# Kernel optimization log

Hardware: AMD Instinct MI355X
Metric: run time of the kernel (lower is better)

## Reference

```python
import math
import jax, jax.numpy as jnp
import numpy as np

D_MODEL = 1024
N_HEAD = 16
HEAD_DIM = D_MODEL // N_HEAD
B, T = 2, 2048


def _layernorm(x, g, b, eps=1e-5):
    mu = jnp.mean(x, axis=-1, keepdims=True)
    var = jnp.mean(jnp.square(x - mu), axis=-1, keepdims=True)
    return (x - mu) * jax.lax.rsqrt(var + eps) * g + b


def _l2norm(x, eps=1e-12):
    n = jnp.sqrt(jnp.sum(jnp.square(x), axis=-1, keepdims=True))
    return x / jnp.maximum(n, eps)


def _rope(x, times):
    # x: [B,T,H,Dh] (Dh even), times: [T]
    half = x.shape[-1] // 2
    freqs = jnp.exp(-jnp.arange(half, dtype=x.dtype) * (math.log(10000.0) / half))
    theta = times[:, None] * freqs[None, :]              # [T, half]
    cos = jnp.cos(theta)[None, :, None, :]               # [1,T,1,half]
    sin = jnp.sin(theta)[None, :, None, :]
    xr = x.reshape(*x.shape[:-1], half, 2)
    x1, x2 = xr[..., 0], xr[..., 1]
    r1 = x1 * cos - x2 * sin
    r2 = x1 * sin + x2 * cos
    return jnp.stack([r1, r2], axis=-1).reshape(x.shape)


def setup_inputs() -> dict:
    key = jax.random.key(0)
    ks = jax.random.split(key, 16)
    s = 0.02
    f32 = jnp.float32
    inp = {
        'x': jax.random.normal(ks[0], (B, T, D_MODEL), f32),
        'Wq': jax.random.normal(ks[1], (D_MODEL, D_MODEL), f32) * s,
        'Wk': jax.random.normal(ks[2], (D_MODEL, D_MODEL), f32) * s,
        'Wv': jax.random.normal(ks[3], (D_MODEL, D_MODEL), f32) * s,
        'gate_w': jax.random.normal(ks[4], (D_MODEL, D_MODEL), f32) * s,
        'gate_b': jnp.zeros((D_MODEL,), f32),
        'p_w': jax.random.normal(ks[5], (D_MODEL, D_MODEL), f32) * s,
        'p_b': jnp.zeros((D_MODEL,), f32),
        'out_w': jax.random.normal(ks[6], (D_MODEL, D_MODEL), f32) * s,
        'out_b': jnp.zeros((D_MODEL,), f32),
        'clock_w': jax.random.normal(ks[7], (D_MODEL, N_HEAD), f32) * s,
        'clock_b': jnp.zeros((N_HEAD,), f32),
        'ln1_g': jnp.ones((D_MODEL,), f32), 'ln1_b': jnp.zeros((D_MODEL,), f32),
        'ln2_g': jnp.ones((D_MODEL,), f32), 'ln2_b': jnp.zeros((D_MODEL,), f32),
        'mlp_w1': jax.random.normal(ks[8], (D_MODEL, 4 * D_MODEL), f32) * s,
        'mlp_b1': jnp.zeros((4 * D_MODEL,), f32),
        'mlp_w2': jax.random.normal(ks[9], (4 * D_MODEL, D_MODEL), f32) * s,
        'mlp_b2': jnp.zeros((D_MODEL,), f32),
    }
    return inp


def reference(x, Wq, Wk, Wv, gate_w, gate_b, p_w, p_b, out_w, out_b,
              clock_w, clock_b, ln1_g, ln1_b, ln2_g, ln2_b,
              mlp_w1, mlp_b1, mlp_w2, mlp_b2):
    Bx, Tx, D = x.shape
    H, Dh = N_HEAD, HEAD_DIM
    residual = x
    xn = _layernorm(x, ln1_g, ln1_b)
    times = jnp.arange(Tx, dtype=x.dtype)

    q = _l2norm((xn @ Wq).reshape(Bx, Tx, H, Dh))
    k = _l2norm((xn @ Wk).reshape(Bx, Tx, H, Dh))
    v = (xn @ Wv).reshape(Bx, Tx, H, Dh)
    clock = jax.nn.softplus(xn @ clock_w + clock_b).reshape(Bx, Tx, H, 1)

    q = _rope(q, times)
    k = _rope(k, times)

    gj = -jax.nn.softplus(xn @ gate_w + gate_b).reshape(Bx, Tx, H, Dh)
    gcp = jnp.exp(jnp.clip(jnp.cumsum(gj, axis=1), -60.0, 50.0))
    q = q * gcp
    k = k / (gcp + 1e-8)

    p = (xn @ p_w + p_b).reshape(Bx, Tx, H, Dh)
    p_max = jnp.max(p, axis=1, keepdims=True)
    p_exp = jnp.exp(p - p_max) * clock
    p_cs = jnp.cumsum(p_exp, axis=1)
    q = q / (p_cs + 1e-8)
    k = k * p_exp

    # causal softmax attention (SDPA, scale = 1/sqrt(Dh))
    scores = jnp.einsum('bqhd,bkhd->bhqk', q, k) / math.sqrt(Dh)
    mask = jnp.tril(jnp.ones((Tx, Tx), dtype=bool))
    scores = jnp.where(mask[None, None], scores, -jnp.inf)
    attn = jax.nn.softmax(scores, axis=-1)
    out = jnp.einsum('bhqk,bkhd->bqhd', attn, v).reshape(Bx, Tx, D)

    out = out @ out_w + out_b
    x1 = out + residual
    h = _layernorm(x1, ln2_g, ln2_b)
    h = jax.nn.gelu(h @ mlp_w1 + mlp_b1, approximate=False) @ mlp_w2 + mlp_b2
    return x1 + h
```

## Files before the change

### kernel.cpp

```cpp
#include <hip/hip_runtime.h>
#include <hip/hip_bf16.h>
#include <math.h>

typedef __hip_bfloat16 bf16;
typedef __attribute__((ext_vector_type(8))) short short8;
typedef __attribute__((ext_vector_type(4))) short short4v;
typedef __attribute__((ext_vector_type(4))) float f32x4;

#define BT   4096
#define DM   1024
#define NH   16
#define DH   64
#define TSEQ 2048

__device__ __forceinline__ float wave_sum(float v){
#pragma unroll
  for (int o = 32; o; o >>= 1) v += __shfl_xor(v, o);
  return v;
}

__device__ __forceinline__ float block_sum(float v){
  __shared__ float sm[4];
  v = wave_sum(v);
  __syncthreads();
  if ((threadIdx.x & 63) == 0) sm[threadIdx.x >> 6] = v;
  __syncthreads();
  return sm[0] + sm[1] + sm[2] + sm[3];
}

__device__ __forceinline__ float softplusf(float x){
  return x > 20.f ? x : __logf(1.f + __expf(x));
}

__device__ __forceinline__ short f2bf(float f){
  unsigned u = __builtin_bit_cast(unsigned, f);
  u += 0x7FFF + ((u >> 16) & 1);
  return (short)(u >> 16);
}

__device__ __forceinline__ short8 ld8(const short* p){
  short4v a = *(const short4v*)p;
  short4v b = *(const short4v*)(p + 4);
  short8 r;
  r[0]=a[0]; r[1]=a[1]; r[2]=a[2]; r[3]=a[3];
  r[4]=b[0]; r[5]=b[1]; r[6]=b[2]; r[7]=b[3];
  return r;
}

__device__ __forceinline__ void async16(const short* g, short* l){
  __builtin_amdgcn_global_load_lds(
      (const __attribute__((address_space(1))) void*)g,
      (__attribute__((address_space(3))) void*)l, 16, 0, 0);
}

__device__ __forceinline__ int xcd_swizzle(int lin, int nwg){
  const int q = nwg >> 3, r = nwg & 7;
  const int xcd = lin & 7, i = lin >> 3;
  return (xcd < r ? xcd * (q + 1) : r * (q + 1) + (xcd - r) * q) + i;
}

__device__ __forceinline__ void wt_body(const float* __restrict__ src,
    short* __restrict__ dst, int K, int N){
  __shared__ short T[32][33];
  const int tx = threadIdx.x & 31, ty = threadIdx.x >> 5;
  const int n0 = blockIdx.x << 5, k0 = blockIdx.y << 5;
#pragma unroll
  for (int r = 0; r < 4; r++){
    const int k = k0 + (ty << 2) + r;
    const int n = n0 + tx;
    T[tx][(ty << 2) + r] = (n < N) ? f2bf(src[(long)k * N + n]) : (short)0;
  }
  __syncthreads();
#pragma unroll
  for (int r = 0; r < 4; r++){
    const int n = n0 + (ty << 2) + r;
    if (n < N) dst[(long)n * K + k0 + tx] = T[(ty << 2) + r][tx];
  }
}

__global__ __launch_bounds__(256) void wt_kernel(const float* __restrict__ src,
    short* __restrict__ dst, int K, int N){
  wt_body(src, dst, K, N);
}

__global__ __launch_bounds__(256) void wt6_kernel(
    const float* s0, const float* s1, const float* s2, const float* s3,
    const float* s4, const float* s5,
    short* d0, short* d1, short* d2, short* d3, short* d4, short* d5){
  const float* src; short* dst;
  switch (blockIdx.z){
    case 0: src = s0; dst = d0; break;
    case 1: src = s1; dst = d1; break;
    case 2: src = s2; dst = d2; break;
    case 3: src = s3; dst = d3; break;
    case 4: src = s4; dst = d4; break;
    default: src = s5; dst = d5; break;
  }
  wt_body(src, dst, DM, DM);
}

__global__ __launch_bounds__(256) void biascat_fill(const float* __restrict__ gb,
    const float* __restrict__ pb, const float* __restrict__ cb, float* __restrict__ out){
  const int i = blockIdx.x * 256 + threadIdx.x;
  if (i >= 5136) return;
  float v = 0.f;
  if (i >= 5120) v = cb[i - 5120];
  else if (i >= 4096) v = pb[i - 4096];
  else if (i >= 3072) v = gb[i - 3072];
  out[i] = v;
}

__global__ __launch_bounds__(256) void ln_kernel(const float* __restrict__ xin,
    const float* __restrict__ g, const float* __restrict__ bb, short* __restrict__ out){
  const long row = blockIdx.x;
  const int tid = threadIdx.x;
  float v[4];
#pragma unroll
  for (int i = 0; i < 4; i++) v[i] = xin[row * DM + tid + i * 256];
  float s = block_sum(v[0] + v[1] + v[2] + v[3]);
  const float mu = s * (1.f / DM);
  float d2 = 0.f;
#pragma unroll
  for (int i = 0; i < 4; i++){ float dd = v[i] - mu; d2 = fmaf(dd, dd, d2); }
  d2 = block_sum(d2);
  const float rstd = rsqrtf(d2 * (1.f / DM) + 1e-5f);
#pragma unroll
  for (int i = 0; i < 4; i++){
    int c = tid + i * 256;
    out[row * DM + c] = f2bf(fmaf((v[i] - mu) * rstd, g[c], bb[c]));
  }
}

template <int EPI>
__global__ __launch_bounds__(256) void gemm_bt(
    const short* __restrict__ A, const short* __restrict__ Bt,
    const float* __restrict__ bias, const float* __restrict__ resf,
    const float* __restrict__ bias2, float* __restrict__ Cf2,
    float* __restrict__ Cf, short* __restrict__ Cbf, int M, int N, int K)
{
  __shared__ __attribute__((aligned(16))) short As[3][4096];
  __shared__ __attribute__((aligned(16))) short Bs[3][4096];
  const int tid = threadIdx.x;
  const int lane = tid & 63, w = tid >> 6;
  const int l16 = lane & 15, quad = lane >> 4;
  const int wm = w >> 1, wn = w & 1;
  const int gx = (int)gridDim.x, gy = (int)gridDim.y;
  int wg = xcd_swizzle((int)blockIdx.x + gx * ((int)blockIdx.y + gy * (int)blockIdx.z),
                       gx * gy * (int)gridDim.z);
  const int bx = wg % gx; wg /= gx;
  const int by = wg % gy; wg /= gy;
  const int bz = wg;
  const int bm0 = by << 7, bn0 = bx << 7;
  const int ks = K / (int)gridDim.z;
  const int kbeg = bz * ks;
  const int nt = ks >> 5;

  const int csw = (tid >> 3) & 3;
  const int r0 = tid >> 2,        c0 = (tid & 3) ^ csw;
  const int r1 = 64 + (tid >> 2);
  const short* ga0 = A  + (long)(bm0 + r0) * K + kbeg + c0 * 8;
  const short* ga1 = A  + (long)(bm0 + r1) * K + kbeg + c0 * 8;
  const short* gb0 = Bt + (long)min(bn0 + r0, N - 1) * K + kbeg + c0 * 8;
  const short* gb1 = Bt + (long)min(bn0 + r1, N - 1) * K + kbeg + c0 * 8;
  const int wofs = w << 9;

#define STAGE(buf, t) do {                                   \
    const long ko_ = (long)(t) * 32;                         \
    async16(ga0 + ko_, &As[buf][wofs]);                      \
    async16(gb0 + ko_, &Bs[buf][wofs]);                      \
    async16(ga1 + ko_, &As[buf][2048 + wofs]);               \
    async16(gb1 + ko_, &Bs[buf][2048 + wofs]);               \
  } while (0)

  f32x4 acc[4][4] = {};

  STAGE(0, 0);
  if (nt > 1) STAGE(1, 1);

  const int qsw = (quad ^ ((l16 >> 1) & 3)) * 8;

  int cur = 0, stg = 2;
  for (int t = 0; t < nt; t++){
    if (t + 1 < nt){
      asm volatile("s_waitcnt vmcnt(4)" ::: "memory");
    } else {
      asm volatile("s_waitcnt vmcnt(0)" ::: "memory");
    }
    __builtin_amdgcn_s_barrier();
    __builtin_amdgcn_sched_barrier(0);
    if (t + 2 < nt) STAGE(stg, t + 2);
    short8 af[4], bfr[4];
#pragma unroll
    for (int i = 0; i < 4; i++){
      af[i]  = *(const short8*)&As[cur][(wm * 64 + i * 16 + l16) * 32 + qsw];
      bfr[i] = *(const short8*)&Bs[cur][(wn * 64 + i * 16 + l16) * 32 + qsw];
    }
#pragma unroll
    for (int i = 0; i < 4; i++)
#pragma unroll
      for (int j = 0; j < 4; j++)
        acc[i][j] = __builtin_amdgcn_mfma_f32_16x16x32_bf16(af[i], bfr[j], acc[i][j], 0, 0, 0);
    cur = (cur == 2) ? 0 : cur + 1;
    stg = (stg == 2) ? 0 : stg + 1;
  }
#undef STAGE

#pragma unroll
  for (int i = 0; i < 4; i++){
#pragma unroll
    for (int r = 0; r < 4; r++){
      const int row = bm0 + wm * 64 + i * 16 + quad * 4 + r;
#pragma unroll
      for (int j = 0; j < 4; j++){
        const int col = bn0 + wn * 64 + j * 16 + l16;
        if (col < N){
          float v = acc[i][j][r];
          const long off = (long)row * N + col;
          if constexpr (EPI >= 1 && EPI != 6) v += bias[col];
          if constexpr (EPI == 2 || EPI == 4) v += resf[off];
          if constexpr (EPI == 3){
            v = 0.5f * v * (1.f + erff(v * 0.70710678118654752f));
            Cbf[off] = f2bf(v);
          } else if constexpr (EPI == 4){
            Cf[off] = v;
            Cf2[off] = v + bias2[col];
          } else if constexpr (EPI == 5){
            if (col < 5120)
              Cf[(long)(col >> 10) * 4194304 + (long)row * 1024 + (col & 1023)] = v;
            else
              Cf[20971520 + (long)row * 16 + (col - 5120)] = v;
          } else if constexpr (EPI == 6){
            unsafeAtomicAdd(&Cf[off], v);
          } else {
            Cf[off] = v;
          }
        }
      }
    }
  }
}

__global__ __launch_bounds__(256) void scan_p1(float* __restrict__ G, const float* __restrict__ P,
    const float* __restrict__ Vf, short* __restrict__ Vh,
    float* __restrict__ cmax, float* __restrict__ gsum){
  const int tid = blockIdx.x * 256 + threadIdx.x;
  const int d = tid & 63, c = (tid >> 6) & 31, bh = tid >> 11;
  const int h = bh & 15, b = bh >> 4;
  const long base = (((long)(b * TSEQ + c * 64)) * NH + h) * 64 + d;
  float mx = -1e30f, gs = 0.f;
  for (int tt = 0; tt < 64; tt++){
    const long idx = base + (long)tt * (NH * 64);
    float gj = -softplusf(G[idx]);
    G[idx] = gj;
    gs += gj;
    mx = fmaxf(mx, P[idx]);
    Vh[idx] = f2bf(Vf[idx]);
  }
  const int chain = bh * 64 + d;
  cmax[chain * 32 + c] = mx;
  gsum[chain * 32 + c] = gs;
}

__global__ void scan_p2(const float* __restrict__ cmax, const float* __restrict__ gsum,
                        float* __restrict__ pmax, float* __restrict__ gpre){
  const int chain = blockIdx.x * 256 + threadIdx.x;
  float mx = -1e30f;
  for (int c = 0; c < 32; c++) mx = fmaxf(mx, cmax[chain * 32 + c]);
  pmax[chain] = mx;
  float run = 0.f;
  for (int c = 0; c < 32; c++){ gpre[chain * 32 + c] = run; run += gsum[chain * 32 + c]; }
}

__global__ __launch_bounds__(256) void scan_p3(const float* __restrict__ G, float* __restrict__ P,
    const float* __restrict__ CLKr, float* __restrict__ Q, float* __restrict__ K,
    const float* __restrict__ pmax, const float* __restrict__ gpre, float* __restrict__ psum){
  const int tid = blockIdx.x * 256 + threadIdx.x;
  const int d = tid & 63, c = (tid >> 6) & 31, bh = tid >> 11;
  const int h = bh & 15, b = bh >> 4;
  const int chain = bh * 64 + d;
  const long base = (((long)(b * TSEQ + c * 64)) * NH + h) * 64 + d;
  const float pm = pmax[chain];
  const float freq = expf(-(float)(d >> 1) * 0.28782313662425575f);
  float sn = sinf((float)(c * 64) * freq);
  float cn = cosf((float)(c * 64) * freq);
  const float sf = sinf(freq), cf = cosf(freq);
  float grun = gpre[chain * 32 + c];
  float ps = 0.f;
  for (int tt = 0; tt < 64; tt++){
    const long idx = base + (long)tt * (NH * 64);
    const int t = c * 64 + tt;
    float clk = softplusf(CLKr[(long)(b * TSEQ + t) * NH + h]);
    float pe = __expf(P[idx] - pm) * clk;
    P[idx] = pe; ps += pe;
    grun += G[idx];
    float gc = __expf(fminf(fmaxf(grun, -60.f), 50.f));
    {
      float q = Q[idx];
      float n = sqrtf(wave_sum(q * q));
      q = q / fmaxf(n, 1e-12f);
      float pr = __shfl_xor(q, 1);
      q = (d & 1) ? fmaf(pr, sn, q * cn) : fmaf(q, cn, -pr * sn);
      Q[idx] = q * gc;
    }
    {
      float k = K[idx];
      float n = sqrtf(wave_sum(k * k));
      k = k / fmaxf(n, 1e-12f);
      float pr = __shfl_xor(k, 1);
      k = (d & 1) ? fmaf(pr, sn, k * cn) : fmaf(k, cn, -pr * sn);
      K[idx] = k / (gc + 1e-8f);
    }
    const float ns = fmaf(sn, cf, cn * sf);
    const float nc = fmaf(cn, cf, -sn * sf);
    sn = ns; cn = nc;
  }
  psum[chain * 32 + c] = ps;
}

__global__ void scan_p4(const float* __restrict__ psum, float* __restrict__ ppre){
  const int chain = blockIdx.x * 256 + threadIdx.x;
  float run = 0.f;
  for (int c = 0; c < 32; c++){ ppre[chain * 32 + c] = run; run += psum[chain * 32 + c]; }
}

__global__ __launch_bounds__(256) void scan_p5(const float* __restrict__ P, const float* __restrict__ Q,
    const float* __restrict__ K, const float* __restrict__ ppre,
    short* __restrict__ Qh, short* __restrict__ Kh){
  const int tid = blockIdx.x * 256 + threadIdx.x;
  const int d = tid & 63, c = (tid >> 6) & 31, bh = tid >> 11;
  const int h = bh & 15, b = bh >> 4;
  const int chain = bh * 64 + d;
  const long base = (((long)(b * TSEQ + c * 64)) * NH + h) * 64 + d;
  float cs = ppre[chain * 32 + c];
  for (int tt = 0; tt < 64; tt++){
    const long idx = base + (long)tt * (NH * 64);
    float pe = P[idx];
    cs += pe;
    Qh[idx] = f2bf(Q[idx] / (cs + 1e-8f) * 0.125f);
    Kh[idx] = f2bf(K[idx] * pe);
  }
}

__global__ __launch_bounds__(256) void fattn_kernel(const short* __restrict__ Qh,
    const short* __restrict__ Kh, const short* __restrict__ Vh, short* __restrict__ O){
  __shared__ __attribute__((aligned(16))) short Ks[64][72];
  __shared__ __attribute__((aligned(16))) short Vt[64][68];
  __shared__ __attribute__((aligned(16))) short Ps[4][16][72];
  const int tid  = threadIdx.x;
  const int lane = tid & 63, w = tid >> 6;
  const int quad = lane >> 4, l16 = lane & 15;
  const int gx = (int)gridDim.x;
  int wgs = xcd_swizzle((int)blockIdx.x + gx * (int)blockIdx.y, gx * (int)gridDim.y);
  const int bxs = wgs % gx;
  const int bh = wgs / gx, h = bh & 15, b = bh >> 4;
  const int qt = gx - 1 - bxs;
  const int q0  = qt << 6;
  const int qw0 = q0 + w * 16;
  const long strideT = NH * DH;
  const long base_bh = ((long)b * TSEQ * NH + h) * DH;

  const short* qp = Qh + base_bh + (long)(qw0 + l16) * strideT + quad * 8;
  const short8 qa0 = *(const short8*)qp;
  const short8 qa1 = *(const short8*)(qp + 32);

  f32x4 oacc[4] = {{0,0,0,0},{0,0,0,0},{0,0,0,0},{0,0,0,0}};
  float lpart[4] = {0.f,0.f,0.f,0.f};

  const int krow = tid >> 2, kcol = (tid & 3) << 4;
  const int vkey = tid & 63, vd0 = (tid >> 6) << 4;
  const short* kbase = Kh + base_bh + (long)krow * strideT + kcol;
  const short* vbase = Vh + base_bh + (long)vkey * strideT + vd0;

  short8 kr0 = *(const short8*)kbase;
  short8 kr1 = *(const short8*)(kbase + 8);
  short8 vr0 = *(const short8*)vbase;
  short8 vr1 = *(const short8*)(vbase + 8);

  const int ntiles = qt + 1;
  for (int t = 0; t < ntiles; t++){
    *(short8*)&Ks[krow][kcol]     = kr0;
    *(short8*)&Ks[krow][kcol + 8] = kr1;
#pragma unroll
    for (int j = 0; j < 8; j++) Vt[vd0 + j][vkey] = vr0[j];
#pragma unroll
    for (int j = 0; j < 8; j++) Vt[vd0 + 8 + j][vkey] = vr1[j];
    __syncthreads();
    if (t + 1 < ntiles){
      const long off = (long)(t + 1) * (64 * strideT);
      kr0 = *(const short8*)(kbase + off);
      kr1 = *(const short8*)(kbase + off + 8);
      vr0 = *(const short8*)(vbase + off);
      vr1 = *(const short8*)(vbase + off + 8);
    }
    const int kt0 = t << 6;
    f32x4 c[4] = {{0,0,0,0},{0,0,0,0},{0,0,0,0},{0,0,0,0}};
#pragma unroll
    for (int kg = 0; kg < 4; kg++){
      const short8 b0 = ld8(&Ks[kg * 16 + l16][quad * 8]);
      const short8 b1 = ld8(&Ks[kg * 16 + l16][32 + quad * 8]);
      c[kg] = __builtin_amdgcn_mfma_f32_16x16x32_bf16(qa0, b0, c[kg], 0, 0, 0);
      c[kg] = __builtin_amdgcn_mfma_f32_16x16x32_bf16(qa1, b1, c[kg], 0, 0, 0);
    }
    if (kt0 + 63 > qw0){
#pragma unroll
      for (int kg = 0; kg < 4; kg++)
#pragma unroll
        for (int r = 0; r < 4; r++){
          const int qq = qw0 + quad * 4 + r;
          if (kt0 + kg * 16 + l16 > qq) c[kg][r] = -1e30f;
        }
    }
#pragma unroll
    for (int kg = 0; kg < 4; kg++)
#pragma unroll
      for (int r = 0; r < 4; r++) c[kg][r] = __expf(c[kg][r] - 0.25f);
#pragma unroll
    for (int r = 0; r < 4; r++)
      lpart[r] += (c[0][r] + c[1][r]) + (c[2][r] + c[3][r]);
#pragma unroll
    for (int kg = 0; kg < 4; kg++)
#pragma unroll
      for (int r = 0; r < 4; r++)
        Ps[w][quad * 4 + r][kg * 16 + l16] = f2bf(c[kg][r]);
    const short8 pa0 = ld8(&Ps[w][l16][quad * 8]);
    const short8 pa1 = ld8(&Ps[w][l16][32 + quad * 8]);
#pragma unroll
    for (int f = 0; f < 4; f++){
      const short8 vb0 = ld8(&Vt[f * 16 + l16][quad * 8]);
      const short8 vb1 = ld8(&Vt[f * 16 + l16][32 + quad * 8]);
      oacc[f] = __builtin_amdgcn_mfma_f32_16x16x32_bf16(pa0, vb0, oacc[f], 0, 0, 0);
      oacc[f] = __builtin_amdgcn_mfma_f32_16x16x32_bf16(pa1, vb1, oacc[f], 0, 0, 0);
    }
    __syncthreads();
  }
#pragma unroll
  for (int r = 0; r < 4; r++){
    float l = lpart[r];
#pragma unroll
    for (int o = 1; o <= 8; o <<= 1) l += __shfl_xor(l, o);
    const float inv = 1.f / l;
    const long row = base_bh + (long)(qw0 + quad * 4 + r) * strideT + l16;
#pragma unroll
    for (int f = 0; f < 4; f++) O[row + f * 16] = f2bf(oacc[f][r] * inv);
  }
}

extern "C" void kernel_launch(void* const* d_in, const int* in_sizes, int n_in,
                              void* d_out, int out_size, void* d_ws, size_t ws_size,
                              hipStream_t stream){
  const float* x       = (const float*)d_in[0];
  const float* Wq      = (const float*)d_in[1];
  const float* Wk      = (const float*)d_in[2];
  const float* Wv      = (const float*)d_in[3];
  const float* gate_w  = (const float*)d_in[4];
  const float* gate_b  = (const float*)d_in[5];
  const float* p_w     = (const float*)d_in[6];
  const float* p_b     = (const float*)d_in[7];
  const float* out_w   = (const float*)d_in[8];
  const float* out_b   = (const float*)d_in[9];
  const float* clock_w = (const float*)d_in[10];
  const float* clock_b = (const float*)d_in[11];
  const float* ln1_g   = (const float*)d_in[12];
  const float* ln1_b   = (const float*)d_in[13];
  const float* ln2_g   = (const float*)d_in[14];
  const float* ln2_b   = (const float*)d_in[15];
  const float* mlp_w1  = (const float*)d_in[16];
  const float* mlp_b1  = (const float*)d_in[17];
  const float* mlp_w2  = (const float*)d_in[18];
  const float* mlp_b2  = (const float*)d_in[19];
  float* outp = (float*)d_out;

  float* ws   = (float*)d_ws;
  float* C5   = ws;
  float* Qb   = ws;
  float* Kb   = ws + 4194304;
  float* Vf   = ws + 8388608;
  float* Gb   = ws + 12582912;
  float* Pb   = ws + 16777216;
  float* CLKr = ws + 20971520;
  float* cmax = CLKr + 65536;
  float* gsum = cmax + 65536;
  float* gpre = gsum + 65536;
  float* pmax = gpre + 65536;
  float* biascat = cmax;
  short* sb   = (short*)(ws + 21235712);
  short* XNb  = sb;
  short* Vh   = sb;
  short* WcT  = sb + 4194304;
  short* OwT  = WcT + 5260288;
  short* W1T  = OwT + 1048576;
  short* W2T  = W1T + 4194304;
  short* Qh  = (short*)(ws + 8388608);
  short* Kh  = (short*)(ws + 8388608 + 2097152);
  short* MID = (short*)ws;
  short* Ob  = (short*)(ws + 12582912);
  short* Hb  = (short*)(ws + 12582912 + 2097152);
  float* X1  = Pb;

  wt6_kernel<<<dim3(32, 32, 6), 256, 0, stream>>>(
      Wq, Wk, Wv, gate_w, p_w, out_w,
      WcT, WcT + 1048576, WcT + 2097152, WcT + 3145728, WcT + 4194304, OwT);
  wt_kernel<<<dim3(1, 32), 256, 0, stream>>>(clock_w, WcT + 5242880, DM, NH);
  wt_kernel<<<dim3(128, 32), 256, 0, stream>>>(mlp_w1, W1T, DM, 4 * DM);
  wt_kernel<<<dim3(32, 128), 256, 0, stream>>>(mlp_w2, W2T, 4 * DM, DM);
  biascat_fill<<<21, 256, 0, stream>>>(gate_b, p_b, clock_b, biascat);

  ln_kernel<<<BT, 256, 0, stream>>>(x, ln1_g, ln1_b, XNb);

  gemm_bt<5><<<dim3(41, BT / 128), 256, 0, stream>>>(
      XNb, WcT, biascat, nullptr, nullptr, nullptr, C5, nullptr, BT, 5136, DM);

  scan_p1<<<256, 256, 0, stream>>>(Gb, Pb, Vf, Vh, cmax, gsum);
  scan_p2<<<8, 256, 0, stream>>>(cmax, gsum, pmax, gpre);
  scan_p3<<<256, 256, 0, stream>>>(Gb, Pb, CLKr, Qb, Kb, pmax, gpre, gsum);
  scan_p4<<<8, 256, 0, stream>>>(gsum, gpre);
  scan_p5<<<256, 256, 0, stream>>>(Pb, Qb, Kb, gpre, Qh, Kh);

  fattn_kernel<<<dim3(TSEQ / 64, 2 * NH), 256, 0, stream>>>(Qh, Kh, Vh, Ob);

  gemm_bt<4><<<dim3(DM / 128, BT / 128), 256, 0, stream>>>(
      Ob, OwT, out_b, x, mlp_b2, outp, X1, nullptr, BT, DM, DM);
  ln_kernel<<<BT, 256, 0, stream>>>(X1, ln2_g, ln2_b, Hb);
  gemm_bt<3><<<dim3(4 * DM / 128, BT / 128), 256, 0, stream>>>(
      Hb, W1T, mlp_b1, nullptr, nullptr, nullptr, nullptr, MID, BT, 4 * DM, DM);
  gemm_bt<6><<<dim3(DM / 128, BT / 128, 4), 256, 0, stream>>>(
      MID, W2T, nullptr, nullptr, nullptr, nullptr, outp, nullptr, BT, DM, 4 * DM);
}
```

Measured before the change: 636.2 us.

## Add 256x128-tile triple-buffered GEMM for QKV and MLP projections

```diff
diff --git a/kernel.cpp b/kernel.cpp
--- a/kernel.cpp
+++ b/kernel.cpp
@@ -224,6 +224,111 @@
           } else if constexpr (EPI == 4){
             Cf[off] = v;
             Cf2[off] = v + bias2[col];
+          } else if constexpr (EPI == 6){
+            unsafeAtomicAdd(&Cf[off], v);
+          } else {
+            Cf[off] = v;
+          }
+        }
+      }
+    }
+  }
+}
+
+template <int EPI>
+__global__ __launch_bounds__(256, 2) void gemm_bt2(
+    const short* __restrict__ A, const short* __restrict__ Bt,
+    const float* __restrict__ bias, const float* __restrict__ resf,
+    float* __restrict__ Cf, short* __restrict__ Cbf, int M, int N, int K)
+{
+  __shared__ __attribute__((aligned(16))) short As[3][8192];
+  __shared__ __attribute__((aligned(16))) short Bs[3][4096];
+  const int tid = threadIdx.x;
+  const int lane = tid & 63, w = tid >> 6;
+  const int l16 = lane & 15, quad = lane >> 4;
+  const int wm = w >> 1, wn = w & 1;
+  const int gx = (int)gridDim.x, gy = (int)gridDim.y;
+  int wg = xcd_swizzle((int)blockIdx.x + gx * ((int)blockIdx.y + gy * (int)blockIdx.z),
+                       gx * gy * (int)gridDim.z);
+  const int bx = wg % gx; wg /= gx;
+  const int by = wg % gy; wg /= gy;
+  const int bz = wg;
+  const int bm0 = by << 8, bn0 = bx << 7;
+  const int ks = K / (int)gridDim.z;
+  const int kbeg = bz * ks;
+  const int nt = ks >> 5;
+
+  const int csw = (tid >> 3) & 3;
+  const int c0 = (tid & 3) ^ csw;
+  const int ra = tid >> 2;
+  const short* ga0 = A  + (long)(bm0 + ra)       * K + kbeg + c0 * 8;
+  const short* ga1 = A  + (long)(bm0 + 64 + ra)  * K + kbeg + c0 * 8;
+  const short* ga2 = A  + (long)(bm0 + 128 + ra) * K + kbeg + c0 * 8;
+  const short* ga3 = A  + (long)(bm0 + 192 + ra) * K + kbeg + c0 * 8;
+  const short* gb0 = Bt + (long)min(bn0 + ra, N - 1)      * K + kbeg + c0 * 8;
+  const short* gb1 = Bt + (long)min(bn0 + 64 + ra, N - 1) * K + kbeg + c0 * 8;
+  const int wofs = w << 9;
+
+#define STAGE2(buf, t) do {                                  \
+    const long ko_ = (long)(t) * 32;                         \
+    async16(ga0 + ko_, &As[buf][wofs]);                      \
+    async16(ga1 + ko_, &As[buf][2048 + wofs]);               \
+    async16(ga2 + ko_, &As[buf][4096 + wofs]);               \
+    async16(ga3 + ko_, &As[buf][6144 + wofs]);               \
+    async16(gb0 + ko_, &Bs[buf][wofs]);                      \
+    async16(gb1 + ko_, &Bs[buf][2048 + wofs]);               \
+  } while (0)
+
+  f32x4 acc[8][4] = {};
+
+  STAGE2(0, 0);
+  if (nt > 1) STAGE2(1, 1);
+
+  const int qsw = (quad ^ ((l16 >> 1) & 3)) * 8;
+
+  int cur = 0, stg = 2;
+  for (int t = 0; t < nt; t++){
+    if (t + 1 < nt){
+      asm volatile("s_waitcnt vmcnt(6)" ::: "memory");
+    } else {
+      asm volatile("s_waitcnt vmcnt(0)" ::: "memory");
+    }
+    __builtin_amdgcn_s_barrier();
+    __builtin_amdgcn_sched_barrier(0);
+    if (t + 2 < nt) STAGE2(stg, t + 2);
+    short8 af[8], bfr[4];
+#pragma unroll
+    for (int i = 0; i < 8; i++)
+      af[i]  = *(const short8*)&As[cur][(wm * 128 + i * 16 + l16) * 32 + qsw];
+#pragma unroll
+    for (int j = 0; j < 4; j++)
+      bfr[j] = *(const short8*)&Bs[cur][(wn * 64 + j * 16 + l16) * 32 + qsw];
+#pragma unroll
+    for (int i = 0; i < 8; i++)
+#pragma unroll
+      for (int j = 0; j < 4; j++)
+        acc[i][j] = __builtin_amdgcn_mfma_f32_16x16x32_bf16(af[i], bfr[j], acc[i][j], 0, 0, 0);
+    cur = (cur == 2) ? 0 : cur + 1;
+    stg = (stg == 2) ? 0 : stg + 1;
+  }
+#undef STAGE2
+
+#pragma unroll
+  for (int i = 0; i < 8; i++){
+#pragma unroll
+    for (int r = 0; r < 4; r++){
+      const int row = bm0 + wm * 128 + i * 16 + quad * 4 + r;
+#pragma unroll
+      for (int j = 0; j < 4; j++){
+        const int col = bn0 + wn * 64 + j * 16 + l16;
+        if (col < N){
+          float v = acc[i][j][r];
+          const long off = (long)row * N + col;
+          if constexpr (EPI >= 1 && EPI != 6) v += bias[col];
+          if constexpr (EPI == 2) v += resf[off];
+          if constexpr (EPI == 3){
+            v = 0.5f * v * (1.f + erff(v * 0.70710678118654752f));
+            Cbf[off] = f2bf(v);
           } else if constexpr (EPI == 5){
             if (col < 5120)
               Cf[(long)(col >> 10) * 4194304 + (long)row * 1024 + (col & 1023)] = v;
@@ -507,8 +612,8 @@
 
   ln_kernel<<<BT, 256, 0, stream>>>(x, ln1_g, ln1_b, XNb);
 
-  gemm_bt<5><<<dim3(41, BT / 128), 256, 0, stream>>>(
-      XNb, WcT, biascat, nullptr, nullptr, nullptr, C5, nullptr, BT, 5136, DM);
+  gemm_bt2<5><<<dim3(41, BT / 256), 256, 0, stream>>>(
+      XNb, WcT, biascat, nullptr, C5, nullptr, BT, 5136, DM);
 
   scan_p1<<<256, 256, 0, stream>>>(Gb, Pb, Vf, Vh, cmax, gsum);
   scan_p2<<<8, 256, 0, stream>>>(cmax, gsum, pmax, gpre);
@@ -521,8 +626,8 @@
   gemm_bt<4><<<dim3(DM / 128, BT / 128), 256, 0, stream>>>(
       Ob, OwT, out_b, x, mlp_b2, outp, X1, nullptr, BT, DM, DM);
   ln_kernel<<<BT, 256, 0, stream>>>(X1, ln2_g, ln2_b, Hb);
-  gemm_bt<3><<<dim3(4 * DM / 128, BT / 128), 256, 0, stream>>>(
-      Hb, W1T, mlp_b1, nullptr, nullptr, nullptr, nullptr, MID, BT, 4 * DM, DM);
-  gemm_bt<6><<<dim3(DM / 128, BT / 128, 4), 256, 0, stream>>>(
-      MID, W2T, nullptr, nullptr, nullptr, nullptr, outp, nullptr, BT, DM, 4 * DM);
-}
+  gemm_bt2<3><<<dim3(4 * DM / 128, BT / 256), 256, 0, stream>>>(
+      Hb, W1T, mlp_b1, nullptr, nullptr, MID, BT, 4 * DM, DM);
+  gemm_bt2<6><<<dim3(DM / 128, BT / 256, 4), 256, 0, stream>>>(
+      MID, W2T, nullptr, nullptr, outp, nullptr, BT, DM, 4 * DM);
+}
```

Result: no change. 644.1 us (+1.2%).
